# Optimization experiments

Measured on AMD Instinct MI355X. Metric: run time of the kernel, lower is better.

The kernel has to match this reference:

```python
import jax, jax.numpy as jnp
import numpy as np

B, T, V, E, H = 4096, 128, 30, 256, 128

def setup_inputs() -> dict:
    key = jax.random.key(0)
    ks = jax.random.split(key, 12)
    inpt = jax.random.randint(ks[0], (B, T), 0, V, dtype=jnp.int32)
    h0 = jax.random.normal(ks[1], (B, H), dtype=jnp.float32)
    c0 = jax.random.normal(ks[2], (B, H), dtype=jnp.float32)
    mask_Y = jnp.ones((B, T), dtype=jnp.float32)
    s_e = 1.0
    s_l = 1.0 / np.sqrt(H)
    s_i = 1.0 / np.sqrt(E)
    emb = jax.random.normal(ks[3], (V, E), dtype=jnp.float32) * s_e
    W_ih = jax.random.normal(ks[4], (4 * H, E), dtype=jnp.float32) * s_i
    b_ih = jax.random.normal(ks[5], (4 * H,), dtype=jnp.float32) * s_i
    W_hh = jax.random.normal(ks[6], (4 * H, H), dtype=jnp.float32) * s_l
    b_hh = jax.random.normal(ks[7], (4 * H,), dtype=jnp.float32) * s_l
    W_lin = jax.random.normal(ks[8], (V, H), dtype=jnp.float32) * s_l
    b_lin = jax.random.normal(ks[9], (V,), dtype=jnp.float32) * s_l
    return {"inpt": inpt, "h0": h0, "c0": c0, "mask_Y": mask_Y, "beta": 1,
            "emb": emb, "W_ih": W_ih, "b_ih": b_ih, "W_hh": W_hh,
            "b_hh": b_hh, "W_lin": W_lin, "b_lin": b_lin}


def reference(inpt, h0, c0, mask_Y, beta, emb, W_ih, b_ih, W_hh, b_hh, W_lin, b_lin):
    # beta == 1 -> teacher forcing every step (u <= beta always), as in source.
    t_max = inpt.shape[1]
    # input tokens fed at steps t=0..t_max-2 are inpt[:, 0:t_max-1]
    x_emb = emb[inpt[:, :t_max - 1]]          # [B, T-1, E]
    xs = (jnp.swapaxes(x_emb, 0, 1),           # [T-1, B, E]
          inpt[:, 1:].T,                       # [T-1, B] true labels
          mask_Y[:, :t_max - 1].T)             # [T-1, B]

    def step(carry, xs_t):
        h, c = carry
        x, y, m = xs_t
        gates = x @ W_ih.T + b_ih + h @ W_hh.T + b_hh   # [B, 4H]
        i, f, g, o = jnp.split(gates, 4, axis=1)
        c2 = jax.nn.sigmoid(f) * c + jax.nn.sigmoid(i) * jnp.tanh(g)
        h2 = jax.nn.sigmoid(o) * jnp.tanh(c2)
        # -log(softmax(logits))[y] == -log_softmax(logits)[y]
        logp = jax.nn.log_softmax(h2 @ W_lin.T + b_lin, axis=1)  # [B, V]
        ce = -jnp.take_along_axis(logp, y[:, None], axis=1)[:, 0]
        return (h2, c2), jnp.sum(ce * m)

    _, step_losses = jax.lax.scan(step, (h0, c0), xs)
    return jnp.sum(step_losses) / jnp.sum(mask_Y)
```

## Files before the change

kernel.cpp:

```cpp
#include <hip/hip_runtime.h>


typedef __bf16 bf16x8 __attribute__((ext_vector_type(8)));
typedef float  f32x4  __attribute__((ext_vector_type(4)));

namespace {
constexpr int Bn = 4096, Tn = 128, Vn = 30, En = 256, Hn = 128, Gn = 512;
constexpr int WS_LOSS  = 0;
constexpr int WS_MASK  = 1;
constexpr int WS_CNT   = 2;
constexpr int WS_XPROJ = 16;
constexpr int WS_WF_F  = WS_XPROJ + Vn * Gn;
}

__device__ __forceinline__ float fexp2(float x) { return __builtin_amdgcn_exp2f(x); }
__device__ __forceinline__ float frcp(float x)  { return __builtin_amdgcn_rcpf(x); }
__device__ __forceinline__ float sigf(float x)  { return frcp(1.f + fexp2(x * -1.44269504f)); }
__device__ __forceinline__ float tanh_(float x) { return 1.f - 2.f * frcp(fexp2(x * 2.88539008f) + 1.f); }

__global__ void k_setup(const float* __restrict__ emb, const float* __restrict__ W_ih,
                        const float* __restrict__ b_ih, const float* __restrict__ b_hh,
                        const float* __restrict__ W_hh, const float* __restrict__ W_lin,
                        float* __restrict__ ws) {
  const int bid = blockIdx.x, tid = threadIdx.x;
  if (bid < 60) {
    __shared__ __align__(16) float es[En];
    int v = bid >> 1;
    int j = ((bid & 1) << 8) + tid;
    es[tid] = emb[v * En + tid];
    __syncthreads();
    float a = b_ih[j] + b_hh[j];
    const float* wr = W_ih + j * En;
#pragma unroll 4
    for (int e = 0; e < En; e += 4) {
      float4 w = *(const float4*)(wr + e);
      float4 x = *(const float4*)(es + e);
      a += x.x * w.x + x.y * w.y + x.z * w.z + x.w * w.w;
    }
    ws[WS_XPROJ + v * Gn + (j & 127) * 4 + (j >> 7)] = a;
  } else if (bid < 92) {
    int fid = (bid - 60) * 256 + tid;
    int l = fid & 63, kt = (fid >> 6) & 3, g = (fid >> 8) & 3, w = fid >> 10;
    int n  = (g * 8 + w) * 16 + (l & 15);
    int k0 = kt * 32 + (l >> 4) * 8;
    const float* src = W_hh + n * Hn + k0;
    union { __bf16 h[8]; uint4 u; } pk;
#pragma unroll
    for (int j = 0; j < 8; ++j) pk.h[j] = (__bf16)src[j];
    __bf16* wf = (__bf16*)(ws + WS_WF_F);
    *(uint4*)(wf + fid * 8) = pk.u;
  } else {
    int fid = (bid - 92) * 256 + tid;
    if (fid < 3) ws[fid] = 0.f;
    int l = fid & 63, kt = (fid >> 6) & 3, n = fid >> 8;
    int col = n * 16 + (l & 15);
    int k0  = kt * 32 + (l >> 4) * 8;
    union { __bf16 h[8]; uint4 u; } pk;
#pragma unroll
    for (int j = 0; j < 8; ++j)
      pk.h[j] = (col < Vn) ? (__bf16)W_lin[col * Hn + k0 + j] : (__bf16)0.f;
    __bf16* wf = (__bf16*)(ws + WS_WF_F);
    *(uint4*)(wf + 65536 + fid * 8) = pk.u;
  }
}

__global__ __launch_bounds__(576, 1) void k_main(
    const int* __restrict__ inpt, const float* __restrict__ h0,
    const float* __restrict__ c0, const float* __restrict__ maskY,
    const float* __restrict__ b_lin, float* __restrict__ ws,
    float* __restrict__ out) {
  __shared__ __align__(16) __bf16 hbuf[2][16][136];
  __shared__ int   tokL[16 * 129];
  __shared__ float maskL[16 * 132];
  __shared__ __align__(16) float logits[16 * 36];
  __shared__ float red[2];

  const float4* X4 = (const float4*)(ws + WS_XPROJ);
  const __bf16* wf = (const __bf16*)(ws + WS_WF_F);
  const __bf16* wlf = wf + 65536;

  const int tid = threadIdx.x;
  const int w = tid >> 6, l = tid & 63, quad = l >> 4, lc = l & 15;
  const int row0 = blockIdx.x * 16;
  const int kh = w * 16 + lc;

  for (int idx = tid; idx < 16 * Tn; idx += 576) {
    int r = idx >> 7, t = idx & 127;
    tokL[r * 129 + t]  = inpt[(row0 + r) * Tn + t];
    maskL[r * 132 + t] = maskY[(row0 + r) * Tn + t];
  }
  for (int idx = tid; idx < 16 * Hn; idx += 576) {
    int r = idx >> 7, k = idx & 127;
    hbuf[0][r][k] = (__bf16)h0[(row0 + r) * Hn + k];
  }

  bf16x8 wreg[4][4];
  float  creg[4];
  float  bias0 = 0.f, bias1 = 0.f, mloc = 0.f;
  if (w < 8) {
#pragma unroll
    for (int g = 0; g < 4; ++g)
#pragma unroll
      for (int kt = 0; kt < 4; ++kt)
        wreg[g][kt] = __builtin_bit_cast(
            bf16x8, *(const uint4*)(wf + (((w * 4 + g) * 4 + kt) * 64 + l) * 8));
#pragma unroll
    for (int p = 0; p < 4; ++p)
      creg[p] = c0[(row0 + quad * 4 + p) * Hn + kh];
    if (w == 7) {
      float s = 0.f;
      const float4* m4 = (const float4*)(maskY + row0 * Tn);
#pragma unroll
      for (int i = 0; i < 8; ++i) s += m4[l + i * 64].x + m4[l + i * 64].y +
                                       m4[l + i * 64].z + m4[l + i * 64].w;
      mloc = s;
    }
  } else {
#pragma unroll
    for (int n = 0; n < 2; ++n)
#pragma unroll
      for (int kt = 0; kt < 4; ++kt)
        wreg[n][kt] = __builtin_bit_cast(
            bf16x8, *(const uint4*)(wlf + ((n * 4 + kt) * 64 + l) * 8));
    bias0 = b_lin[lc];
    bias1 = (lc < Vn - 16) ? b_lin[lc + 16] : -1e30f;
  }
  float ce_acc = 0.f;
  __syncthreads();

  float4 xv[4];
  if (w < 8) {
#pragma unroll
    for (int p = 0; p < 4; ++p)
      xv[p] = X4[tokL[(quad * 4 + p) * 129] * 128 + kh];
  }

  for (int t = 0; t < Tn; ++t) {
    const int par = t & 1;
    const __bf16* hc = &hbuf[par][0][0];
    __bf16*       hn = &hbuf[par ^ 1][0][0];

    if (w < 8) {
      if (t < Tn - 1) {
        bf16x8 af[4];
#pragma unroll
        for (int kt = 0; kt < 4; ++kt)
          af[kt] = __builtin_bit_cast(
              bf16x8, *(const uint4*)(hc + lc * 136 + kt * 32 + quad * 8));

        int tk[4];
#pragma unroll
        for (int p = 0; p < 4; ++p) tk[p] = tokL[(quad * 4 + p) * 129 + t + 1];

        f32x4 acc[4];
#pragma unroll
        for (int p = 0; p < 4; ++p) {
          acc[0][p] = xv[p].x; acc[1][p] = xv[p].y;
          acc[2][p] = xv[p].z; acc[3][p] = xv[p].w;
        }
#pragma unroll
        for (int g = 0; g < 4; ++g)
#pragma unroll
          for (int kt = 0; kt < 4; ++kt)
            acc[g] = __builtin_amdgcn_mfma_f32_16x16x32_bf16(af[kt], wreg[g][kt], acc[g], 0, 0, 0);

        float4 xn[4];
#pragma unroll
        for (int p = 0; p < 4; ++p) xn[p] = X4[tk[p] * 128 + kh];

#pragma unroll
        for (int p = 0; p < 4; ++p) {
          float c2 = sigf(acc[1][p]) * creg[p] + sigf(acc[0][p]) * tanh_(acc[2][p]);
          float h2 = sigf(acc[3][p]) * tanh_(c2);
          creg[p] = c2;
          hn[(quad * 4 + p) * 136 + kh] = (__bf16)h2;
          xv[p] = xn[p];
        }
      }
    } else if (t >= 1) {
      bf16x8 af[4];
#pragma unroll
      for (int kt = 0; kt < 4; ++kt)
        af[kt] = __builtin_bit_cast(
            bf16x8, *(const uint4*)(hc + lc * 136 + kt * 32 + quad * 8));
      f32x4 lacc[2] = {{bias0, bias0, bias0, bias0}, {bias1, bias1, bias1, bias1}};
#pragma unroll
      for (int kt = 0; kt < 4; ++kt) {
        lacc[0] = __builtin_amdgcn_mfma_f32_16x16x32_bf16(af[kt], wreg[0][kt], lacc[0], 0, 0, 0);
        lacc[1] = __builtin_amdgcn_mfma_f32_16x16x32_bf16(af[kt], wreg[1][kt], lacc[1], 0, 0, 0);
      }
#pragma unroll
      for (int p = 0; p < 4; ++p) {
        logits[(quad * 4 + p) * 36 + lc]      = lacc[0][p];
        logits[(quad * 4 + p) * 36 + 16 + lc] = lacc[1][p];
      }
      int row = l >> 2, j = l & 3;
      float4 v0 = *(const float4*)(logits + row * 36 + j * 8);
      float4 v1 = *(const float4*)(logits + row * 36 + j * 8 + 4);
      float m = fmaxf(fmaxf(fmaxf(v0.x, v0.y), fmaxf(v0.z, v0.w)),
                      fmaxf(fmaxf(v1.x, v1.y), fmaxf(v1.z, v1.w)));
      m = fmaxf(m, __shfl_xor(m, 1));
      m = fmaxf(m, __shfl_xor(m, 2));
      float e = fexp2((v0.x - m) * 1.44269504f) + fexp2((v0.y - m) * 1.44269504f) +
                fexp2((v0.z - m) * 1.44269504f) + fexp2((v0.w - m) * 1.44269504f) +
                fexp2((v1.x - m) * 1.44269504f) + fexp2((v1.y - m) * 1.44269504f) +
                fexp2((v1.z - m) * 1.44269504f) + fexp2((v1.w - m) * 1.44269504f);
      e += __shfl_xor(e, 1);
      e += __shfl_xor(e, 2);
      if (j == 0) {
        int   y  = tokL[row * 129 + t];
        float ly = logits[row * 36 + y];
        float ce = (m + __logf(e)) - ly;
        ce_acc += ce * maskL[row * 132 + t - 1];
      }
    }
    __syncthreads();
  }

  if (w == 7) {
#pragma unroll
    for (int off = 32; off > 0; off >>= 1) mloc += __shfl_down(mloc, off);
    if (l == 0) red[0] = mloc;
  }
  __syncthreads();
  if (w == 8) {
#pragma unroll
    for (int off = 32; off > 0; off >>= 1) ce_acc += __shfl_down(ce_acc, off);
    if (l == 0) {
      atomicAdd(ws + WS_LOSS, ce_acc);
      atomicAdd(ws + WS_MASK, red[0]);
      __threadfence();
      unsigned old = atomicAdd((unsigned*)(ws + WS_CNT), 1u);
      if (old == 255) {
        float lv = atomicAdd(ws + WS_LOSS, 0.f);
        float mv = atomicAdd(ws + WS_MASK, 0.f);
        out[0] = lv / mv;
      }
    }
  }
}

extern "C" void kernel_launch(void* const* d_in, const int* in_sizes, int n_in,
                              void* d_out, int out_size, void* d_ws, size_t ws_size,
                              hipStream_t stream) {
  const int*   inpt  = (const int*)  d_in[0];
  const float* h0    = (const float*)d_in[1];
  const float* c0    = (const float*)d_in[2];
  const float* maskY = (const float*)d_in[3];
  const float* emb   = (const float*)d_in[5];
  const float* W_ih  = (const float*)d_in[6];
  const float* b_ih  = (const float*)d_in[7];
  const float* W_hh  = (const float*)d_in[8];
  const float* b_hh  = (const float*)d_in[9];
  const float* W_lin = (const float*)d_in[10];
  const float* b_lin = (const float*)d_in[11];
  float* ws  = (float*)d_ws;
  float* out = (float*)d_out;

  hipLaunchKernelGGL(k_setup, dim3(94),  dim3(256), 0, stream,
                     emb, W_ih, b_ih, b_hh, W_hh, W_lin, ws);
  hipLaunchKernelGGL(k_main,  dim3(256), dim3(576), 0, stream,
                     inpt, h0, c0, maskY, b_lin, ws, out);
}
```

Before: 228.5 us.

## Transpose MFMA layout, rotate softmax across four waves, fuse gate math

```diff
diff --git a/kernel.cpp b/kernel.cpp
--- a/kernel.cpp
+++ b/kernel.cpp
@@ -15,8 +15,6 @@
 
 __device__ __forceinline__ float fexp2(float x) { return __builtin_amdgcn_exp2f(x); }
 __device__ __forceinline__ float frcp(float x)  { return __builtin_amdgcn_rcpf(x); }
-__device__ __forceinline__ float sigf(float x)  { return frcp(1.f + fexp2(x * -1.44269504f)); }
-__device__ __forceinline__ float tanh_(float x) { return 1.f - 2.f * frcp(fexp2(x * 2.88539008f) + 1.f); }
 
 __global__ void k_setup(const float* __restrict__ emb, const float* __restrict__ W_ih,
                         const float* __restrict__ b_ih, const float* __restrict__ b_hh,
@@ -40,8 +38,8 @@
     ws[WS_XPROJ + v * Gn + (j & 127) * 4 + (j >> 7)] = a;
   } else if (bid < 92) {
     int fid = (bid - 60) * 256 + tid;
-    int l = fid & 63, kt = (fid >> 6) & 3, g = (fid >> 8) & 3, w = fid >> 10;
-    int n  = (g * 8 + w) * 16 + (l & 15);
+    int l = fid & 63, kt = (fid >> 6) & 3, T = (fid >> 8) & 3, w = fid >> 10;
+    int n  = (l & 3) * 128 + w * 16 + T * 4 + ((l >> 2) & 3);
     int k0 = kt * 32 + (l >> 4) * 8;
     const float* src = W_hh + n * Hn + k0;
     union { __bf16 h[8]; uint4 u; } pk;
@@ -52,19 +50,19 @@
   } else {
     int fid = (bid - 92) * 256 + tid;
     if (fid < 3) ws[fid] = 0.f;
-    int l = fid & 63, kt = (fid >> 6) & 3, n = fid >> 8;
-    int col = n * 16 + (l & 15);
-    int k0  = kt * 32 + (l >> 4) * 8;
+    int l = fid & 63, kt = (fid >> 6) & 3, T = fid >> 8;
+    int vocab = T * 16 + (l & 15);
+    int k0 = kt * 32 + (l >> 4) * 8;
     union { __bf16 h[8]; uint4 u; } pk;
 #pragma unroll
     for (int j = 0; j < 8; ++j)
-      pk.h[j] = (col < Vn) ? (__bf16)W_lin[col * Hn + k0 + j] : (__bf16)0.f;
+      pk.h[j] = (vocab < Vn) ? (__bf16)W_lin[vocab * Hn + k0 + j] : (__bf16)0.f;
     __bf16* wf = (__bf16*)(ws + WS_WF_F);
     *(uint4*)(wf + 65536 + fid * 8) = pk.u;
   }
 }
 
-__global__ __launch_bounds__(576, 1) void k_main(
+__global__ __launch_bounds__(768, 3) void k_main(
     const int* __restrict__ inpt, const float* __restrict__ h0,
     const float* __restrict__ c0, const float* __restrict__ maskY,
     const float* __restrict__ b_lin, float* __restrict__ ws,
@@ -72,41 +70,40 @@
   __shared__ __align__(16) __bf16 hbuf[2][16][136];
   __shared__ int   tokL[16 * 129];
   __shared__ float maskL[16 * 132];
-  __shared__ __align__(16) float logits[16 * 36];
-  __shared__ float red[2];
 
   const float4* X4 = (const float4*)(ws + WS_XPROJ);
-  const __bf16* wf = (const __bf16*)(ws + WS_WF_F);
+  const __bf16* wf  = (const __bf16*)(ws + WS_WF_F);
   const __bf16* wlf = wf + 65536;
 
   const int tid = threadIdx.x;
   const int w = tid >> 6, l = tid & 63, quad = l >> 4, lc = l & 15;
   const int row0 = blockIdx.x * 16;
-  const int kh = w * 16 + lc;
-
-  for (int idx = tid; idx < 16 * Tn; idx += 576) {
+
+  for (int idx = tid; idx < 16 * Tn; idx += 768) {
     int r = idx >> 7, t = idx & 127;
     tokL[r * 129 + t]  = inpt[(row0 + r) * Tn + t];
     maskL[r * 132 + t] = maskY[(row0 + r) * Tn + t];
   }
-  for (int idx = tid; idx < 16 * Hn; idx += 576) {
+  for (int idx = tid; idx < 16 * Hn; idx += 768) {
     int r = idx >> 7, k = idx & 127;
     hbuf[0][r][k] = (__bf16)h0[(row0 + r) * Hn + k];
   }
 
   bf16x8 wreg[4][4];
   float  creg[4];
-  float  bias0 = 0.f, bias1 = 0.f, mloc = 0.f;
+  float  blin[2][4];
+  float  mloc = 0.f, ce_acc = 0.f;
+
   if (w < 8) {
 #pragma unroll
-    for (int g = 0; g < 4; ++g)
+    for (int T = 0; T < 4; ++T)
 #pragma unroll
       for (int kt = 0; kt < 4; ++kt)
-        wreg[g][kt] = __builtin_bit_cast(
-            bf16x8, *(const uint4*)(wf + (((w * 4 + g) * 4 + kt) * 64 + l) * 8));
-#pragma unroll
-    for (int p = 0; p < 4; ++p)
-      creg[p] = c0[(row0 + quad * 4 + p) * Hn + kh];
+        wreg[T][kt] = __builtin_bit_cast(
+            bf16x8, *(const uint4*)(wf + (((w * 4 + T) * 4 + kt) * 64 + l) * 8));
+#pragma unroll
+    for (int T = 0; T < 4; ++T)
+      creg[T] = c0[(row0 + lc) * Hn + w * 16 + T * 4 + quad];
     if (w == 7) {
       float s = 0.f;
       const float4* m4 = (const float4*)(maskY + row0 * Tn);
@@ -117,102 +114,120 @@
     }
   } else {
 #pragma unroll
-    for (int n = 0; n < 2; ++n)
+    for (int T = 0; T < 2; ++T)
 #pragma unroll
       for (int kt = 0; kt < 4; ++kt)
-        wreg[n][kt] = __builtin_bit_cast(
-            bf16x8, *(const uint4*)(wlf + ((n * 4 + kt) * 64 + l) * 8));
-    bias0 = b_lin[lc];
-    bias1 = (lc < Vn - 16) ? b_lin[lc + 16] : -1e30f;
-  }
-  float ce_acc = 0.f;
+        wreg[T][kt] = __builtin_bit_cast(
+            bf16x8, *(const uint4*)(wlf + ((T * 4 + kt) * 64 + l) * 8));
+#pragma unroll
+    for (int T = 0; T < 2; ++T)
+#pragma unroll
+      for (int r = 0; r < 4; ++r) {
+        int vo = T * 16 + quad * 4 + r;
+        blin[T][r] = (vo < Vn) ? b_lin[vo] : -1e30f;
+      }
+  }
   __syncthreads();
+
+  const int toff = lc * 129;
+  const int moff = lc * 132;
+  const int aoff = lc * 136 + quad * 8;
+  const int woff = lc * 136 + w * 16 + quad;
 
   float4 xv[4];
   if (w < 8) {
-#pragma unroll
-    for (int p = 0; p < 4; ++p)
-      xv[p] = X4[tokL[(quad * 4 + p) * 129] * 128 + kh];
+    int tok = tokL[toff];
+    const float4* xb = X4 + tok * 128 + w * 16 + quad;
+#pragma unroll
+    for (int T = 0; T < 4; ++T) xv[T] = xb[T * 4];
   }
 
   for (int t = 0; t < Tn; ++t) {
-    const int par = t & 1;
-    const __bf16* hc = &hbuf[par][0][0];
-    __bf16*       hn = &hbuf[par ^ 1][0][0];
+    const __bf16* hc = &hbuf[t & 1][0][0];
+    __bf16*       hn = &hbuf[(t & 1) ^ 1][0][0];
 
     if (w < 8) {
       if (t < Tn - 1) {
         bf16x8 af[4];
 #pragma unroll
         for (int kt = 0; kt < 4; ++kt)
-          af[kt] = __builtin_bit_cast(
-              bf16x8, *(const uint4*)(hc + lc * 136 + kt * 32 + quad * 8));
-
-        int tk[4];
-#pragma unroll
-        for (int p = 0; p < 4; ++p) tk[p] = tokL[(quad * 4 + p) * 129 + t + 1];
+          af[kt] = __builtin_bit_cast(bf16x8, *(const uint4*)(hc + aoff + kt * 32));
+        int tok = tokL[toff + t + 1];
 
         f32x4 acc[4];
 #pragma unroll
-        for (int p = 0; p < 4; ++p) {
-          acc[0][p] = xv[p].x; acc[1][p] = xv[p].y;
-          acc[2][p] = xv[p].z; acc[3][p] = xv[p].w;
-        }
-#pragma unroll
-        for (int g = 0; g < 4; ++g)
+        for (int T = 0; T < 4; ++T) acc[T] = __builtin_bit_cast(f32x4, xv[T]);
+#pragma unroll
+        for (int T = 0; T < 4; ++T)
 #pragma unroll
           for (int kt = 0; kt < 4; ++kt)
-            acc[g] = __builtin_amdgcn_mfma_f32_16x16x32_bf16(af[kt], wreg[g][kt], acc[g], 0, 0, 0);
+            acc[T] = __builtin_amdgcn_mfma_f32_16x16x32_bf16(wreg[T][kt], af[kt], acc[T], 0, 0, 0);
 
         float4 xn[4];
-#pragma unroll
-        for (int p = 0; p < 4; ++p) xn[p] = X4[tk[p] * 128 + kh];
-
-#pragma unroll
-        for (int p = 0; p < 4; ++p) {
-          float c2 = sigf(acc[1][p]) * creg[p] + sigf(acc[0][p]) * tanh_(acc[2][p]);
-          float h2 = sigf(acc[3][p]) * tanh_(c2);
-          creg[p] = c2;
-          hn[(quad * 4 + p) * 136 + kh] = (__bf16)h2;
-          xv[p] = xn[p];
+        const float4* xb = X4 + tok * 128 + w * 16 + quad;
+#pragma unroll
+        for (int T = 0; T < 4; ++T) xn[T] = xb[T * 4];
+
+#pragma unroll
+        for (int T = 0; T < 4; ++T) {
+          float iv = acc[T][0], fv = acc[T][1], gv = acc[T][2], ov = acc[T][3];
+          float ef = fexp2(fv * -1.44269504f);
+          float ei = fexp2(iv * -1.44269504f);
+          float eo = fexp2(ov * -1.44269504f);
+          float eg = fexp2(fminf(gv, 16.f) * 2.88539008f);
+          float sf = frcp(1.f + ef);
+          float itg = (eg - 1.f) * frcp((1.f + ei) * (1.f + eg));
+          float c2 = sf * creg[T] + itg;
+          float ec = fexp2(fminf(c2, 16.f) * 2.88539008f);
+          float h2 = (ec - 1.f) * frcp((1.f + eo) * (1.f + ec));
+          creg[T] = c2;
+          xv[T] = xn[T];
+          hn[woff + T * 4] = (__bf16)h2;
         }
       }
-    } else if (t >= 1) {
+    } else if (t >= 1 && (w - 8) == ((t - 1) & 3)) {
       bf16x8 af[4];
 #pragma unroll
       for (int kt = 0; kt < 4; ++kt)
-        af[kt] = __builtin_bit_cast(
-            bf16x8, *(const uint4*)(hc + lc * 136 + kt * 32 + quad * 8));
-      f32x4 lacc[2] = {{bias0, bias0, bias0, bias0}, {bias1, bias1, bias1, bias1}};
-#pragma unroll
-      for (int kt = 0; kt < 4; ++kt) {
-        lacc[0] = __builtin_amdgcn_mfma_f32_16x16x32_bf16(af[kt], wreg[0][kt], lacc[0], 0, 0, 0);
-        lacc[1] = __builtin_amdgcn_mfma_f32_16x16x32_bf16(af[kt], wreg[1][kt], lacc[1], 0, 0, 0);
+        af[kt] = __builtin_bit_cast(bf16x8, *(const uint4*)(hc + aoff + kt * 32));
+      f32x4 lacc[2];
+#pragma unroll
+      for (int T = 0; T < 2; ++T)
+#pragma unroll
+        for (int r = 0; r < 4; ++r) lacc[T][r] = blin[T][r];
+#pragma unroll
+      for (int T = 0; T < 2; ++T)
+#pragma unroll
+        for (int kt = 0; kt < 4; ++kt)
+          lacc[T] = __builtin_amdgcn_mfma_f32_16x16x32_bf16(wreg[T][kt], af[kt], lacc[T], 0, 0, 0);
+
+      float m = lacc[0][0];
+#pragma unroll
+      for (int T = 0; T < 2; ++T)
+#pragma unroll
+        for (int r = 0; r < 4; ++r) m = fmaxf(m, lacc[T][r]);
+      m = fmaxf(m, __shfl_xor(m, 16));
+      m = fmaxf(m, __shfl_xor(m, 32));
+      float e = 0.f;
+#pragma unroll
+      for (int T = 0; T < 2; ++T)
+#pragma unroll
+        for (int r = 0; r < 4; ++r) e += fexp2((lacc[T][r] - m) * 1.44269504f);
+      e += __shfl_xor(e, 16);
+      e += __shfl_xor(e, 32);
+      int y = tokL[toff + t];
+      float cand = 0.f;
+#pragma unroll
+      for (int T = 0; T < 2; ++T)
+#pragma unroll
+        for (int r = 0; r < 4; ++r)
+          cand = ((T * 16 + quad * 4 + r) == y) ? lacc[T][r] : cand;
+      cand += __shfl_xor(cand, 16);
+      cand += __shfl_xor(cand, 32);
+      if (quad == 0) {
+        float ce = (m + __logf(e)) - cand;
+        ce_acc += ce * maskL[moff + t - 1];
       }
-#pragma unroll
-      for (int p = 0; p < 4; ++p) {
-        logits[(quad * 4 + p) * 36 + lc]      = lacc[0][p];
-        logits[(quad * 4 + p) * 36 + 16 + lc] = lacc[1][p];
-      }
-      int row = l >> 2, j = l & 3;
-      float4 v0 = *(const float4*)(logits + row * 36 + j * 8);
-      float4 v1 = *(const float4*)(logits + row * 36 + j * 8 + 4);
-      float m = fmaxf(fmaxf(fmaxf(v0.x, v0.y), fmaxf(v0.z, v0.w)),
-                      fmaxf(fmaxf(v1.x, v1.y), fmaxf(v1.z, v1.w)));
-      m = fmaxf(m, __shfl_xor(m, 1));
-      m = fmaxf(m, __shfl_xor(m, 2));
-      float e = fexp2((v0.x - m) * 1.44269504f) + fexp2((v0.y - m) * 1.44269504f) +
-                fexp2((v0.z - m) * 1.44269504f) + fexp2((v0.w - m) * 1.44269504f) +
-                fexp2((v1.x - m) * 1.44269504f) + fexp2((v1.y - m) * 1.44269504f) +
-                fexp2((v1.z - m) * 1.44269504f) + fexp2((v1.w - m) * 1.44269504f);
-      e += __shfl_xor(e, 1);
-      e += __shfl_xor(e, 2);
-      if (j == 0) {
-        int   y  = tokL[row * 129 + t];
-        float ly = logits[row * 36 + y];
-        float ce = (m + __logf(e)) - ly;
-        ce_acc += ce * maskL[row * 132 + t - 1];
-      }
     }
     __syncthreads();
   }
@@ -220,22 +235,21 @@
   if (w == 7) {
 #pragma unroll
     for (int off = 32; off > 0; off >>= 1) mloc += __shfl_down(mloc, off);
-    if (l == 0) red[0] = mloc;
+    if (l == 0) atomicAdd(ws + WS_MASK, mloc);
+  }
+  if (w >= 8) {
+#pragma unroll
+    for (int off = 32; off > 0; off >>= 1) ce_acc += __shfl_down(ce_acc, off);
+    if (l == 0) atomicAdd(ws + WS_LOSS, ce_acc);
   }
   __syncthreads();
-  if (w == 8) {
-#pragma unroll
-    for (int off = 32; off > 0; off >>= 1) ce_acc += __shfl_down(ce_acc, off);
-    if (l == 0) {
-      atomicAdd(ws + WS_LOSS, ce_acc);
-      atomicAdd(ws + WS_MASK, red[0]);
-      __threadfence();
-      unsigned old = atomicAdd((unsigned*)(ws + WS_CNT), 1u);
-      if (old == 255) {
-        float lv = atomicAdd(ws + WS_LOSS, 0.f);
-        float mv = atomicAdd(ws + WS_MASK, 0.f);
-        out[0] = lv / mv;
-      }
+  if (tid == 0) {
+    __threadfence();
+    unsigned old = atomicAdd((unsigned*)(ws + WS_CNT), 1u);
+    if (old == 255) {
+      float lv = atomicAdd(ws + WS_LOSS, 0.f);
+      float mv = atomicAdd(ws + WS_MASK, 0.f);
+      out[0] = lv / mv;
     }
   }
 }
@@ -259,6 +273,6 @@
 
   hipLaunchKernelGGL(k_setup, dim3(94),  dim3(256), 0, stream,
                      emb, W_ih, b_ih, b_hh, W_hh, W_lin, ws);
-  hipLaunchKernelGGL(k_main,  dim3(256), dim3(576), 0, stream,
+  hipLaunchKernelGGL(k_main,  dim3(256), dim3(768), 0, stream,
                      inpt, h0, c0, maskY, b_lin, ws, out);
 }
```

New measurement: 239.6 us. 1.05x slower.
